# Kernel tuning notes

Hardware: AMD Instinct MI355X
Metric: run time of the kernel (lower is better)

## Reference

```python
import jax, jax.numpy as jnp
import numpy as np

BN_EPS = 1e-5
DIST_EPS = 1e-8
K = 3  # fixed 3-NN interpolation


def _cond_conv(x, t_embed, w_t, b_t, w_c, b_c, gamma, beta):
    # time conditioning: GELU(t) -> Linear -> add to channels
    te = jax.nn.gelu(t_embed, approximate=False) @ w_t.T + b_t  # (B, Cin)
    x = x + te[:, :, None]
    # kernel-size-1 Conv1d == channel GEMM
    x = jnp.einsum('oc,bcn->bon', w_c, x) + b_c[None, :, None]
    # BatchNorm1d, training mode: biased stats over (batch, length)
    m = jnp.mean(x, axis=(0, 2), keepdims=True)
    v = jnp.var(x, axis=(0, 2), keepdims=True)
    x = gamma[None, :, None] * (x - m) * jax.lax.rsqrt(v + BN_EPS) + beta[None, :, None]
    return jax.nn.gelu(x, approximate=False)


def _forward(xyz1, xyz2, points1, points2, t_embed,
             w_t1, b_t1, w_c1, b_c1, g1, be1,
             w_t2, b_t2, w_c2, b_c2, g2, be2):
    # squared euclidean distances (cdist**2), computed directly
    # d2[b,n,s] = ||xyz1[b,n]||^2 + ||xyz2[b,s]||^2 - 2 <xyz1[b,n], xyz2[b,s]>
    n1 = jnp.sum(xyz1 * xyz1, axis=-1)  # (B,N)
    n2 = jnp.sum(xyz2 * xyz2, axis=-1)  # (B,S)
    d2 = n1[:, :, None] + n2[:, None, :] - 2.0 * jnp.einsum('bnc,bsc->bns', xyz1, xyz2)
    # top-3 smallest distances (instead of wasteful full sort)
    neg, idx = jax.lax.top_k(-d2, K)        # (B,N,3)
    dists = -neg
    dist_recip = 1.0 / (dists + DIST_EPS)
    weight = dist_recip / jnp.sum(dist_recip, axis=2, keepdims=True)  # (B,N,3)
    pts2t = jnp.transpose(points2, (0, 2, 1))  # (B,S,C2)
    gathered = jax.vmap(lambda p, i: p[i])(pts2t, idx)  # (B,N,3,C2)
    interp = jnp.einsum('bnkc,bnk->bcn', gathered, weight)  # (B,C2,N)
    new_points = jnp.concatenate([points1, interp], axis=1)  # (B,C1+C2,N)
    new_points = _cond_conv(new_points, t_embed, w_t1, b_t1, w_c1, b_c1, g1, be1)
    new_points = _cond_conv(new_points, t_embed, w_t2, b_t2, w_c2, b_c2, g2, be2)
    return new_points


def setup_inputs() -> dict:
    key = jax.random.key(0)
    ks = jax.random.split(key, 12)
    B, N, S, C1, C2, T = 8, 8192, 2048, 128, 256, 256
    Cin = C1 + C2
    s = lambda fan: 1.0 / np.sqrt(fan)
    return {
        'xyz1': jax.random.normal(ks[0], (B, N, 3), jnp.float32),
        'xyz2': jax.random.normal(ks[1], (B, S, 3), jnp.float32),
        'points1': jax.random.normal(ks[2], (B, C1, N), jnp.float32),
        'points2': jax.random.normal(ks[3], (B, C2, S), jnp.float32),
        't_embed': jax.random.normal(ks[4], (B, T), jnp.float32),
        'w_t1': jax.random.normal(ks[5], (Cin, T), jnp.float32) * s(T),
        'b_t1': jnp.zeros((Cin,), jnp.float32),
        'w_c1': jax.random.normal(ks[6], (256, Cin), jnp.float32) * s(Cin),
        'b_c1': jnp.zeros((256,), jnp.float32),
        'g1': jnp.ones((256,), jnp.float32),
        'be1': jnp.zeros((256,), jnp.float32),
        'w_t2': jax.random.normal(ks[7], (256, T), jnp.float32) * s(T),
        'b_t2': jnp.zeros((256,), jnp.float32),
        'w_c2': jax.random.normal(ks[8], (256, 256), jnp.float32) * s(256),
        'b_c2': jnp.zeros((256,), jnp.float32),
        'g2': jnp.ones((256,), jnp.float32),
        'be2': jnp.zeros((256,), jnp.float32),
    }


def reference(xyz1, xyz2, points1, points2, t_embed,
              w_t1, b_t1, w_c1, b_c1, g1, be1,
              w_t2, b_t2, w_c2, b_c2, g2, be2):
    return _forward(xyz1, xyz2, points1, points2, t_embed,
                    w_t1, b_t1, w_c1, b_c1, g1, be1,
                    w_t2, b_t2, w_c2, b_c2, g2, be2)
```

## Files before the change

kernel.cpp:

```cpp
#include <hip/hip_runtime.h>
#include <cfloat>
#include <cmath>

#define B_   8
#define N_   8192
#define S_   2048
#define C1_  128
#define C2_  256
#define T_   256
#define CIN_ 384
#define CO_  256

#define KCH  16
#define KCS  (S_ / KCH)
#define KQB  1024

typedef __attribute__((ext_vector_type(8))) short short8;
typedef __attribute__((ext_vector_type(4))) float f32x4;

__device__ __forceinline__ float bf2f(unsigned short u) {
    union { unsigned int i; float f; } v; v.i = ((unsigned int)u) << 16; return v.f;
}
__device__ __forceinline__ unsigned short f2bf(float f) {
    union { float f; unsigned int i; } v; v.f = f;
    unsigned int i = v.i;
    unsigned int r = i + 0x7FFFu + ((i >> 16) & 1u);
    return (unsigned short)(r >> 16);
}
__device__ __forceinline__ float gelu_f(float x) {
    return 0.5f * x * (1.0f + erff(x * 0.70710678118654752440f));
}
__device__ __forceinline__ void async16(const void* g, void* l) {
    __builtin_amdgcn_global_load_lds((const __attribute__((address_space(1))) void*)g,
                                     (__attribute__((address_space(3))) void*)l, 16, 0, 0);
}

#define OFF_TE1   0u
#define OFF_TE2   16384u
#define OFF_BN1   28672u
#define OFF_BN2   30720u
#define OFF_WC1   1605632u
#define OFF_WC2   1802240u
#define OFF_P2T   2097152u
#define OFF_X1    10485760u
#define OFF_Y     60817408u
#define OFF_PD    OFF_Y
#define OFF_PI    (OFF_Y + 12582912u)
#define OFF_PS    OFF_P2T
#define OFF_PQ    (OFF_P2T + 1048576u)

__global__ __launch_bounds__(256) void prep_kernel(
    const float* __restrict__ w1, const float* __restrict__ w2,
    unsigned short* __restrict__ o1, unsigned short* __restrict__ o2,
    const float* __restrict__ t_embed,
    const float* __restrict__ w_t1, const float* __restrict__ b_t1,
    const float* __restrict__ w_t2, const float* __restrict__ b_t2,
    float* __restrict__ te1, float* __restrict__ te2)
{
    int bx = blockIdx.x, t = threadIdx.x;
    if (bx < 384) {
        int g = bx * 256 + t;
        o1[g] = f2bf(w1[g]);
        if (g < CO_ * CO_) o2[g] = f2bf(w2[g]);
        return;
    }
    __shared__ float gt[T_];
    int b = bx - 384;
    gt[t] = gelu_f(t_embed[b * T_ + t]);
    __syncthreads();
    for (int o = t; o < CIN_ + CO_; o += 256) {
        if (o < CIN_) {
            const float* w = w_t1 + o * T_;
            float s = 0.f;
            for (int k = 0; k < T_; ++k) s += gt[k] * w[k];
            te1[b * CIN_ + o] = s + b_t1[o];
        } else {
            int oo = o - CIN_;
            const float* w = w_t2 + oo * T_;
            float s = 0.f;
            for (int k = 0; k < T_; ++k) s += gt[k] * w[k];
            te2[b * CO_ + oo] = s + b_t2[oo];
        }
    }
}

__global__ __launch_bounds__(256) void knn_part_kernel(
    const float* __restrict__ xyz1, const float* __restrict__ xyz2,
    float* __restrict__ pd, int* __restrict__ pi)
{
    __shared__ float4 sp[KCS];
    int b = blockIdx.z, ch = blockIdx.y, tid = threadIdx.x;
    int s0 = ch * KCS;
    if (tid < KCS) {
        int gs = s0 + tid;
        float x = xyz2[(b * S_ + gs) * 3 + 0];
        float y = xyz2[(b * S_ + gs) * 3 + 1];
        float z = xyz2[(b * S_ + gs) * 3 + 2];
        sp[tid] = make_float4(x, y, z, x * x + y * y + z * z);
    }
    __syncthreads();

    float nx[4], ny[4], nz[4], nn[4];
    float d1[4], d2[4], d3[4];
    int   i1[4], i2[4], i3[4];
    #pragma unroll
    for (int qq = 0; qq < 4; ++qq) {
        int n = blockIdx.x * KQB + qq * 256 + tid;
        float x1 = xyz1[(b * N_ + n) * 3 + 0];
        float y1 = xyz1[(b * N_ + n) * 3 + 1];
        float z1 = xyz1[(b * N_ + n) * 3 + 2];
        nn[qq] = x1 * x1 + y1 * y1 + z1 * z1;
        nx[qq] = -2.0f * x1; ny[qq] = -2.0f * y1; nz[qq] = -2.0f * z1;
        d1[qq] = FLT_MAX; d2[qq] = FLT_MAX; d3[qq] = FLT_MAX;
        i1[qq] = 0; i2[qq] = 0; i3[qq] = 0;
    }

    for (int s = 0; s < KCS; s += 4) {
        #pragma unroll
        for (int u = 0; u < 4; ++u) {
            float4 p = sp[s + u];
            int gi = s0 + s + u;
            #pragma unroll
            for (int qq = 0; qq < 4; ++qq) {
                float d = fmaf(nx[qq], p.x,
                          fmaf(ny[qq], p.y,
                          fmaf(nz[qq], p.z, p.w)));
                bool c1 = d < d1[qq];
                bool c2 = d < d2[qq];
                bool c3 = d < d3[qq];
                float e1 = fminf(d1[qq], d);
                float e2 = __builtin_amdgcn_fmed3f(d1[qq], d2[qq], d);
                float e3 = __builtin_amdgcn_fmed3f(d2[qq], d3[qq], d);
                int u1  = c1 ? i1[qq] : gi;
                int n1i = c1 ? gi : i1[qq];
                int n2i = c2 ? u1 : i2[qq];
                int u2  = c2 ? i2[qq] : gi;
                int n3i = c3 ? u2 : i3[qq];
                d1[qq] = e1; d2[qq] = e2; d3[qq] = e3;
                i1[qq] = n1i; i2[qq] = n2i; i3[qq] = n3i;
            }
        }
    }

    #pragma unroll
    for (int qq = 0; qq < 4; ++qq) {
        int n = blockIdx.x * KQB + qq * 256 + tid;
        size_t pb = (((size_t)b * KCH + ch) * N_ + n) * 3;
        pd[pb + 0] = d1[qq] + nn[qq];
        pd[pb + 1] = d2[qq] + nn[qq];
        pd[pb + 2] = d3[qq] + nn[qq];
        pi[pb + 0] = i1[qq]; pi[pb + 1] = i2[qq]; pi[pb + 2] = i3[qq];
    }
}

__global__ __launch_bounds__(256) void transpose_fused(
    const float* __restrict__ p2, unsigned short* __restrict__ p2t,
    const float* __restrict__ p1, const float* __restrict__ te1,
    unsigned short* __restrict__ X1)
{
    __shared__ unsigned short tile[32][33];
    int bx = blockIdx.x;
    if (bx < 4096) {
        int b = bx >> 9, cy = (bx >> 6) & 7, sx = bx & 63;
        int s0 = sx * 32, c0 = cy * 32;
        #pragma unroll
        for (int j = 0; j < 4; ++j) {
            int c = threadIdx.y + j * 8;
            tile[c][threadIdx.x] = f2bf(p2[((size_t)b * C2_ + c0 + c) * S_ + s0 + threadIdx.x]);
        }
        __syncthreads();
        #pragma unroll
        for (int j = 0; j < 4; ++j) {
            int s = threadIdx.y + j * 8;
            p2t[((size_t)b * S_ + s0 + s) * C2_ + c0 + threadIdx.x] = tile[threadIdx.x][s];
        }
    } else {
        int bz = bx - 4096;
        int b = bz >> 10, cy = (bz >> 8) & 3, nx = bz & 255;
        int n0 = nx * 32, c0 = cy * 32;
        const float* te = te1 + b * CIN_;
        #pragma unroll
        for (int j = 0; j < 4; ++j) {
            int c = threadIdx.y + j * 8;
            tile[c][threadIdx.x] =
                f2bf(p1[((size_t)b * C1_ + c0 + c) * N_ + n0 + threadIdx.x] + te[c0 + c]);
        }
        __syncthreads();
        #pragma unroll
        for (int j = 0; j < 4; ++j) {
            int n = threadIdx.y + j * 8;
            X1[((size_t)b * N_ + n0 + n) * CIN_ + c0 + threadIdx.x] = tile[threadIdx.x][n];
        }
    }
}

__global__ __launch_bounds__(256) void interp2_kernel(
    const float* __restrict__ pd, const int* __restrict__ pi,
    const unsigned short* __restrict__ p2t,
    const float* __restrict__ te1, unsigned short* __restrict__ X1)
{
    __shared__ float spd[KCH][8][3];
    __shared__ int   spi[KCH][8][3];
    __shared__ float ste[C2_];
    int tid = threadIdx.x;
    int b = blockIdx.x >> 10;
    int n0 = (blockIdx.x & 1023) * 8;
    ste[tid] = te1[b * CIN_ + C1_ + tid];
    if (tid < 128) {
        int ch = tid >> 3, r = tid & 7;
        size_t pb = (((size_t)b * KCH + ch) * N_ + n0 + r) * 3;
        spd[ch][r][0] = pd[pb]; spd[ch][r][1] = pd[pb + 1]; spd[ch][r][2] = pd[pb + 2];
    } else {
        int t2 = tid - 128;
        int ch = t2 >> 3, r = t2 & 7;
        size_t pb = (((size_t)b * KCH + ch) * N_ + n0 + r) * 3;
        spi[ch][r][0] = pi[pb]; spi[ch][r][1] = pi[pb + 1]; spi[ch][r][2] = pi[pb + 2];
    }
    __syncthreads();

    int r = tid >> 5;
    int l = tid & 31;
    float d1, d2, d3; int i1, i2, i3;
    if (l < KCH) {
        d1 = spd[l][r][0]; d2 = spd[l][r][1]; d3 = spd[l][r][2];
        i1 = spi[l][r][0]; i2 = spi[l][r][1]; i3 = spi[l][r][2];
    } else {
        d1 = d2 = d3 = FLT_MAX;
        i1 = i2 = i3 = 0x7FFFFFFF;
    }
    #pragma unroll
    for (int m = 1; m <= 8; m <<= 1) {
        float pd1 = __shfl_xor(d1, m), pd2 = __shfl_xor(d2, m), pd3 = __shfl_xor(d3, m);
        int   pi1 = __shfl_xor(i1, m), pi2 = __shfl_xor(i2, m), pi3 = __shfl_xor(i3, m);
        #pragma unroll
        for (int k = 0; k < 3; ++k) {
            float d = (k == 0) ? pd1 : (k == 1) ? pd2 : pd3;
            int   i = (k == 0) ? pi1 : (k == 1) ? pi2 : pi3;
            bool c1 = (d < d1) || (d == d1 && i < i1);
            bool c2 = (d < d2) || (d == d2 && i < i2);
            bool c3 = (d < d3) || (d == d3 && i < i3);
            float e1 = c1 ? d : d1;        int j1 = c1 ? i : i1;
            float e2 = c1 ? d1 : (c2 ? d : d2);
            int   j2 = c1 ? i1 : (c2 ? i : i2);
            float e3 = c2 ? d2 : (c3 ? d : d3);
            int   j3 = c2 ? i2 : (c3 ? i : i3);
            d1 = e1; d2 = e2; d3 = e3; i1 = j1; i2 = j2; i3 = j3;
        }
    }
    int base = threadIdx.x & 32;
    d1 = __shfl(d1, base); d2 = __shfl(d2, base); d3 = __shfl(d3, base);
    i1 = __shfl(i1, base); i2 = __shfl(i2, base); i3 = __shfl(i3, base);
    float r1 = 1.0f / (d1 + 1e-8f);
    float r2 = 1.0f / (d2 + 1e-8f);
    float r3 = 1.0f / (d3 + 1e-8f);
    float rs = 1.0f / (r1 + r2 + r3);
    float w0 = r1 * rs, w1 = r2 * rs, w2 = r3 * rs;

    int gr = (b << 13) + n0 + r;
    int co = l * 8;
    const unsigned short* q0 = p2t + ((size_t)b * S_ + i1) * C2_ + co;
    const unsigned short* q1 = p2t + ((size_t)b * S_ + i2) * C2_ + co;
    const unsigned short* q2 = p2t + ((size_t)b * S_ + i3) * C2_ + co;
    union { short8 v; unsigned short u[8]; } a0, a1, a2, pk;
    a0.v = *(const short8*)q0;
    a1.v = *(const short8*)q1;
    a2.v = *(const short8*)q2;
    #pragma unroll
    for (int jj = 0; jj < 8; ++jj) {
        float v = w0 * bf2f(a0.u[jj]) + w1 * bf2f(a1.u[jj]) + w2 * bf2f(a2.u[jj])
                + ste[co + jj];
        pk.u[jj] = f2bf(v);
    }
    *(short8*)&X1[(size_t)gr * CIN_ + C1_ + co] = pk.v;
}

template <int K, int MODE>
__global__ __launch_bounds__(256) void gemm_bt(
    const unsigned short* __restrict__ A,
    const unsigned short* __restrict__ X,
    const float* __restrict__ bias,
    unsigned short* __restrict__ out,
    float* __restrict__ psum, float* __restrict__ psq)
{
    __shared__ unsigned short sA[128 * 64];
    __shared__ unsigned short sB[128 * 64];
    const int tid = threadIdx.x;
    const int lane = tid & 63, wave = tid >> 6;
    const int wo = wave >> 1, wm = wave & 1;
    const int quad = lane >> 4, col = lane & 15;
    const int b = blockIdx.z;
    const int x = blockIdx.x;
    const int perm = (x & 7) * 16 + (x >> 3);
    const int n_t = perm >> 1, o_t = perm & 1;
    const int o0 = o_t * 128;
    const int n0 = n_t * 128;
    const unsigned short* Xb = X + (size_t)b * N_ * K;
    const int prow = ((b << 6) + n_t) * 2 + wm;

    f32x4 acc[4][4];
    #pragma unroll
    for (int i = 0; i < 4; ++i)
        #pragma unroll
        for (int j = 0; j < 4; ++j) acc[i][j] = (f32x4){0.f, 0.f, 0.f, 0.f};

    for (int k0 = 0; k0 < K; k0 += 64) {
        #pragma unroll
        for (int i = 0; i < 4; ++i) {
            int chunk = i * 256 + tid;
            int row = chunk >> 3, c8 = chunk & 7;
            async16(&A [(o0 + row) * K + k0 + c8 * 8], &sA[chunk * 8]);
            async16(&Xb[(size_t)(n0 + row) * K + k0 + c8 * 8], &sB[chunk * 8]);
        }
        __syncthreads();
        #pragma unroll
        for (int kk = 0; kk < 64; kk += 32) {
            short8 af[4], bfr[4];
            #pragma unroll
            for (int i = 0; i < 4; ++i)
                af[i] = *(const short8*)&sA[(wo * 64 + i * 16 + col) * 64 + kk + quad * 8];
            #pragma unroll
            for (int j = 0; j < 4; ++j)
                bfr[j] = *(const short8*)&sB[(wm * 64 + j * 16 + col) * 64 + kk + quad * 8];
            #pragma unroll
            for (int i = 0; i < 4; ++i)
                #pragma unroll
                for (int j = 0; j < 4; ++j)
                    acc[i][j] = __builtin_amdgcn_mfma_f32_16x16x32_bf16(af[i], bfr[j], acc[i][j], 0, 0, 0);
        }
        __syncthreads();
    }

    #pragma unroll
    for (int i = 0; i < 4; ++i) {
        int oo = o0 + wo * 64 + i * 16 + quad * 4;
        float bv0 = bias[oo + 0], bv1 = bias[oo + 1];
        float bv2 = bias[oo + 2], bv3 = bias[oo + 3];
        float s0 = 0.f, s1 = 0.f, s2 = 0.f, s3 = 0.f;
        float q0 = 0.f, q1 = 0.f, q2 = 0.f, q3 = 0.f;
        #pragma unroll
        for (int j = 0; j < 4; ++j) {
            int nn = n0 + wm * 64 + j * 16 + col;
            float v0 = acc[i][j][0] + bv0, v1 = acc[i][j][1] + bv1;
            float v2 = acc[i][j][2] + bv2, v3 = acc[i][j][3] + bv3;
            s0 += v0; q0 += v0 * v0; s1 += v1; q1 += v1 * v1;
            s2 += v2; q2 += v2 * v2; s3 += v3; q3 += v3 * v3;
            if (MODE == 0) {
                union { unsigned short u[4]; uint2 p; } pk;
                pk.u[0] = f2bf(v0); pk.u[1] = f2bf(v1);
                pk.u[2] = f2bf(v2); pk.u[3] = f2bf(v3);
                *(uint2*)&out[((size_t)b * N_ + nn) * CO_ + oo] = pk.p;
            } else {
                out[((size_t)b * CO_ + oo + 0) * N_ + nn] = f2bf(v0);
                out[((size_t)b * CO_ + oo + 1) * N_ + nn] = f2bf(v1);
                out[((size_t)b * CO_ + oo + 2) * N_ + nn] = f2bf(v2);
                out[((size_t)b * CO_ + oo + 3) * N_ + nn] = f2bf(v3);
            }
        }
        #pragma unroll
        for (int off = 1; off < 16; off <<= 1) {
            s0 += __shfl_down(s0, off); q0 += __shfl_down(q0, off);
            s1 += __shfl_down(s1, off); q1 += __shfl_down(q1, off);
            s2 += __shfl_down(s2, off); q2 += __shfl_down(q2, off);
            s3 += __shfl_down(s3, off); q3 += __shfl_down(q3, off);
        }
        if (col == 0) {
            float* ps = psum + (size_t)oo * 1024 + prow;
            float* pq = psq  + (size_t)oo * 1024 + prow;
            ps[0] = s0; ps[1024] = s1; ps[2048] = s2; ps[3072] = s3;
            pq[0] = q0; pq[1024] = q1; pq[2048] = q2; pq[3072] = q3;
        }
    }
}

__global__ __launch_bounds__(256) void bn_reduce_kernel(
    const float* __restrict__ psum, const float* __restrict__ psq,
    const float* __restrict__ gamma, const float* __restrict__ beta,
    float* __restrict__ scale, float* __restrict__ shift)
{
    int ch = blockIdx.x * 8 + (threadIdx.x >> 5);
    int l = threadIdx.x & 31;
    float s = 0.f, q = 0.f;
    for (int r = l; r < 1024; r += 32) {
        s += psum[(size_t)ch * 1024 + r];
        q += psq [(size_t)ch * 1024 + r];
    }
    #pragma unroll
    for (int off = 16; off > 0; off >>= 1) {
        s += __shfl_down(s, off, 32);
        q += __shfl_down(q, off, 32);
    }
    if (l == 0) {
        const float inv = 1.0f / 65536.0f;
        float m = s * inv;
        float var = fmaxf(q * inv - m * m, 0.f);
        float sc = gamma[ch] / sqrtf(var + 1e-5f);
        scale[ch] = sc;
        shift[ch] = beta[ch] - m * sc;
    }
}

__global__ __launch_bounds__(256) void apply1_kernel(
    unsigned short* __restrict__ y, const float* __restrict__ scale,
    const float* __restrict__ shift, const float* __restrict__ te2)
{
    __shared__ float ssc[CO_], ssh[CO_], ste[CO_];
    int b = blockIdx.x >> 10;
    int t = threadIdx.x;
    ssc[t] = scale[t]; ssh[t] = shift[t]; ste[t] = te2[b * CO_ + t];
    __syncthreads();
    int g = blockIdx.x * 256 + t;
    int row = g >> 5;
    int og = (g & 31) * 8;
    unsigned short* p = y + (size_t)row * CO_ + og;
    union { short8 v; unsigned short u[8]; } in, op;
    in.v = *(short8*)p;
    #pragma unroll
    for (int jj = 0; jj < 8; ++jj) {
        int o = og + jj;
        op.u[jj] = f2bf(gelu_f(ssc[o] * bf2f(in.u[jj]) + ssh[o]) + ste[o]);
    }
    *(short8*)p = op.v;
}

__global__ __launch_bounds__(256) void final_kernel(
    const unsigned short* __restrict__ z, const float* __restrict__ scale,
    const float* __restrict__ shift, float* __restrict__ out)
{
    int g = blockIdx.x * 256 + threadIdx.x;
    size_t e = (size_t)g * 8;
    int row = (int)(e >> 13);
    int o = row & (CO_ - 1);
    float sc = scale[o], sh = shift[o];
    union { short8 v; unsigned short u[8]; } in;
    in.v = *(const short8*)&z[e];
    float vo[8];
    #pragma unroll
    for (int jj = 0; jj < 8; ++jj)
        vo[jj] = gelu_f(sc * bf2f(in.u[jj]) + sh);
    *(float4*)&out[e]     = make_float4(vo[0], vo[1], vo[2], vo[3]);
    *(float4*)&out[e + 4] = make_float4(vo[4], vo[5], vo[6], vo[7]);
}

extern "C" void kernel_launch(void* const* d_in, const int* in_sizes, int n_in,
                              void* d_out, int out_size, void* d_ws, size_t ws_size,
                              hipStream_t stream)
{
    (void)in_sizes; (void)n_in; (void)out_size; (void)ws_size;
    const float* xyz1    = (const float*)d_in[0];
    const float* xyz2    = (const float*)d_in[1];
    const float* points1 = (const float*)d_in[2];
    const float* points2 = (const float*)d_in[3];
    const float* t_embed = (const float*)d_in[4];
    const float* w_t1    = (const float*)d_in[5];
    const float* b_t1    = (const float*)d_in[6];
    const float* w_c1    = (const float*)d_in[7];
    const float* b_c1    = (const float*)d_in[8];
    const float* g1      = (const float*)d_in[9];
    const float* be1     = (const float*)d_in[10];
    const float* w_t2    = (const float*)d_in[11];
    const float* b_t2    = (const float*)d_in[12];
    const float* w_c2    = (const float*)d_in[13];
    const float* b_c2    = (const float*)d_in[14];
    const float* g2      = (const float*)d_in[15];
    const float* be2     = (const float*)d_in[16];

    char* w = (char*)d_ws;
    float* te1        = (float*)(w + OFF_TE1);
    float* te2        = (float*)(w + OFF_TE2);
    float* scale1     = (float*)(w + OFF_BN1);
    float* shift1     = scale1 + 256;
    float* scale2     = (float*)(w + OFF_BN2);
    float* shift2     = scale2 + 256;
    unsigned short* wc1 = (unsigned short*)(w + OFF_WC1);
    unsigned short* wc2 = (unsigned short*)(w + OFF_WC2);
    unsigned short* p2t = (unsigned short*)(w + OFF_P2T);
    float* pd         = (float*)(w + OFF_PD);
    int*   pi         = (int*)(w + OFF_PI);
    float* psum       = (float*)(w + OFF_PS);
    float* psq        = (float*)(w + OFF_PQ);
    unsigned short* X1  = (unsigned short*)(w + OFF_X1);
    unsigned short* Z   = (unsigned short*)(w + OFF_X1);
    unsigned short* Y   = (unsigned short*)(w + OFF_Y);
    float* out = (float*)d_out;

    hipLaunchKernelGGL(prep_kernel, dim3(392), dim3(256), 0, stream,
                       w_c1, w_c2, wc1, wc2, t_embed, w_t1, b_t1, w_t2, b_t2, te1, te2);
    hipLaunchKernelGGL(knn_part_kernel, dim3(N_ / KQB, KCH, B_), dim3(256), 0, stream,
                       xyz1, xyz2, pd, pi);
    hipLaunchKernelGGL(transpose_fused, dim3(12288), dim3(32, 8), 0, stream,
                       points2, p2t, points1, te1, X1);
    hipLaunchKernelGGL(interp2_kernel, dim3(B_ * N_ / 8), dim3(256), 0, stream,
                       pd, pi, p2t, te1, X1);
    hipLaunchKernelGGL((gemm_bt<CIN_, 0>), dim3(128, 1, B_), dim3(256), 0, stream,
                       wc1, X1, b_c1, Y, psum, psq);
    hipLaunchKernelGGL(bn_reduce_kernel, dim3(32), dim3(256), 0, stream,
                       psum, psq, g1, be1, scale1, shift1);
    hipLaunchKernelGGL(apply1_kernel, dim3(8192), dim3(256), 0, stream,
                       Y, scale1, shift1, te2);
    hipLaunchKernelGGL((gemm_bt<CO_, 1>), dim3(128, 1, B_), dim3(256), 0, stream,
                       wc2, Y, b_c2, Z, psum, psq);
    hipLaunchKernelGGL(bn_reduce_kernel, dim3(32), dim3(256), 0, stream,
                       psum, psq, g2, be2, scale2, shift2);
    hipLaunchKernelGGL(final_kernel, dim3(8192), dim3(256), 0, stream,
                       Z, scale2, shift2, out);
}
```

Before: 347.5 us.

## Fuse BN1-apply/GELU into second GEMM B-load and retune KNN partitioning

Removes the standalone apply1 kernel and instead applies BN1 scale/shift, GELU and the time embedding while staging Y tiles into shared memory inside a new gemm2_fused kernel. This drops one full read and write pass over the intermediate activation. It also halves the KNN split count and the queries per block, which shrinks the partial top-3 buffers and merge shuffles, and swaps the med3 builtin for inline asm. In exchange, the B operand now loads synchronously with per-element erf work in the GEMM loop, and GELU is recomputed once for each of the two output-channel tiles.

```diff
diff --git a/kernel.cpp b/kernel.cpp
--- a/kernel.cpp
+++ b/kernel.cpp
@@ -11,9 +11,9 @@
 #define CIN_ 384
 #define CO_  256
 
-#define KCH  16
+#define KCH  8
 #define KCS  (S_ / KCH)
-#define KQB  1024
+#define KQB  512
 
 typedef __attribute__((ext_vector_type(8))) short short8;
 typedef __attribute__((ext_vector_type(4))) float f32x4;
@@ -33,6 +33,11 @@
 __device__ __forceinline__ void async16(const void* g, void* l) {
     __builtin_amdgcn_global_load_lds((const __attribute__((address_space(1))) void*)g,
                                      (__attribute__((address_space(3))) void*)l, 16, 0, 0);
+}
+__device__ __forceinline__ float med3f(float a, float b, float c) {
+    float r;
+    asm("v_med3_f32 %0, %1, %2, %3" : "=v"(r) : "v"(a), "v"(b), "v"(c));
+    return r;
 }
 
 #define OFF_TE1   0u
@@ -45,7 +50,7 @@
 #define OFF_X1    10485760u
 #define OFF_Y     60817408u
 #define OFF_PD    OFF_Y
-#define OFF_PI    (OFF_Y + 12582912u)
+#define OFF_PI    (OFF_Y + 6291456u)
 #define OFF_PS    OFF_P2T
 #define OFF_PQ    (OFF_P2T + 1048576u)
 
@@ -91,7 +96,7 @@
     __shared__ float4 sp[KCS];
     int b = blockIdx.z, ch = blockIdx.y, tid = threadIdx.x;
     int s0 = ch * KCS;
-    if (tid < KCS) {
+    {
         int gs = s0 + tid;
         float x = xyz2[(b * S_ + gs) * 3 + 0];
         float y = xyz2[(b * S_ + gs) * 3 + 1];
@@ -100,11 +105,11 @@
     }
     __syncthreads();
 
-    float nx[4], ny[4], nz[4], nn[4];
-    float d1[4], d2[4], d3[4];
-    int   i1[4], i2[4], i3[4];
-    #pragma unroll
-    for (int qq = 0; qq < 4; ++qq) {
+    float nx[2], ny[2], nz[2], nn[2];
+    float d1[2], d2[2], d3[2];
+    int   i1[2], i2[2], i3[2];
+    #pragma unroll
+    for (int qq = 0; qq < 2; ++qq) {
         int n = blockIdx.x * KQB + qq * 256 + tid;
         float x1 = xyz1[(b * N_ + n) * 3 + 0];
         float y1 = xyz1[(b * N_ + n) * 3 + 1];
@@ -121,7 +126,7 @@
             float4 p = sp[s + u];
             int gi = s0 + s + u;
             #pragma unroll
-            for (int qq = 0; qq < 4; ++qq) {
+            for (int qq = 0; qq < 2; ++qq) {
                 float d = fmaf(nx[qq], p.x,
                           fmaf(ny[qq], p.y,
                           fmaf(nz[qq], p.z, p.w)));
@@ -129,8 +134,8 @@
                 bool c2 = d < d2[qq];
                 bool c3 = d < d3[qq];
                 float e1 = fminf(d1[qq], d);
-                float e2 = __builtin_amdgcn_fmed3f(d1[qq], d2[qq], d);
-                float e3 = __builtin_amdgcn_fmed3f(d2[qq], d3[qq], d);
+                float e2 = med3f(d1[qq], d2[qq], d);
+                float e3 = med3f(d2[qq], d3[qq], d);
                 int u1  = c1 ? i1[qq] : gi;
                 int n1i = c1 ? gi : i1[qq];
                 int n2i = c2 ? u1 : i2[qq];
@@ -143,7 +148,7 @@
     }
 
     #pragma unroll
-    for (int qq = 0; qq < 4; ++qq) {
+    for (int qq = 0; qq < 2; ++qq) {
         int n = blockIdx.x * KQB + qq * 256 + tid;
         size_t pb = (((size_t)b * KCH + ch) * N_ + n) * 3;
         pd[pb + 0] = d1[qq] + nn[qq];
@@ -206,12 +211,12 @@
     int b = blockIdx.x >> 10;
     int n0 = (blockIdx.x & 1023) * 8;
     ste[tid] = te1[b * CIN_ + C1_ + tid];
-    if (tid < 128) {
+    if (tid < 64) {
         int ch = tid >> 3, r = tid & 7;
         size_t pb = (((size_t)b * KCH + ch) * N_ + n0 + r) * 3;
         spd[ch][r][0] = pd[pb]; spd[ch][r][1] = pd[pb + 1]; spd[ch][r][2] = pd[pb + 2];
-    } else {
-        int t2 = tid - 128;
+    } else if (tid < 128) {
+        int t2 = tid - 64;
         int ch = t2 >> 3, r = t2 & 7;
         size_t pb = (((size_t)b * KCH + ch) * N_ + n0 + r) * 3;
         spi[ch][r][0] = pi[pb]; spi[ch][r][1] = pi[pb + 1]; spi[ch][r][2] = pi[pb + 2];
@@ -229,7 +234,7 @@
         i1 = i2 = i3 = 0x7FFFFFFF;
     }
     #pragma unroll
-    for (int m = 1; m <= 8; m <<= 1) {
+    for (int m = 1; m <= 4; m <<= 1) {
         float pd1 = __shfl_xor(d1, m), pd2 = __shfl_xor(d2, m), pd3 = __shfl_xor(d3, m);
         int   pi1 = __shfl_xor(i1, m), pi2 = __shfl_xor(i2, m), pi3 = __shfl_xor(i3, m);
         #pragma unroll
@@ -372,6 +377,116 @@
     }
 }
 
+__global__ __launch_bounds__(256) void gemm2_fused(
+    const unsigned short* __restrict__ A,
+    const unsigned short* __restrict__ Y,
+    const float* __restrict__ bias,
+    const float* __restrict__ scale1, const float* __restrict__ shift1,
+    const float* __restrict__ te2,
+    unsigned short* __restrict__ out,
+    float* __restrict__ psum, float* __restrict__ psq)
+{
+    const int K = CO_;
+    __shared__ unsigned short sA[128 * 64];
+    __shared__ unsigned short sB[128 * 64];
+    __shared__ float ssc[CO_], ssh[CO_], ste[CO_];
+    const int tid = threadIdx.x;
+    const int lane = tid & 63, wave = tid >> 6;
+    const int wo = wave >> 1, wm = wave & 1;
+    const int quad = lane >> 4, col = lane & 15;
+    const int b = blockIdx.z;
+    const int x = blockIdx.x;
+    const int perm = (x & 7) * 16 + (x >> 3);
+    const int n_t = perm >> 1, o_t = perm & 1;
+    const int o0 = o_t * 128;
+    const int n0 = n_t * 128;
+    const unsigned short* Yb = Y + (size_t)b * N_ * K;
+    const int prow = ((b << 6) + n_t) * 2 + wm;
+
+    ssc[tid] = scale1[tid]; ssh[tid] = shift1[tid]; ste[tid] = te2[b * CO_ + tid];
+    __syncthreads();
+
+    f32x4 acc[4][4];
+    #pragma unroll
+    for (int i = 0; i < 4; ++i)
+        #pragma unroll
+        for (int j = 0; j < 4; ++j) acc[i][j] = (f32x4){0.f, 0.f, 0.f, 0.f};
+
+    for (int k0 = 0; k0 < K; k0 += 64) {
+        #pragma unroll
+        for (int i = 0; i < 4; ++i) {
+            int chunk = i * 256 + tid;
+            int row = chunk >> 3, c8 = chunk & 7;
+            async16(&A[(o0 + row) * K + k0 + c8 * 8], &sA[chunk * 8]);
+        }
+        #pragma unroll
+        for (int i = 0; i < 4; ++i) {
+            int chunk = i * 256 + tid;
+            int row = chunk >> 3, c8 = chunk & 7;
+            int cbase = k0 + c8 * 8;
+            union { short8 v; unsigned short u[8]; } raw, pk;
+            raw.v = *(const short8*)&Yb[(size_t)(n0 + row) * K + cbase];
+            #pragma unroll
+            for (int jj = 0; jj < 8; ++jj) {
+                int c = cbase + jj;
+                pk.u[jj] = f2bf(gelu_f(ssc[c] * bf2f(raw.u[jj]) + ssh[c]) + ste[c]);
+            }
+            *(short8*)&sB[chunk * 8] = pk.v;
+        }
+        __syncthreads();
+        #pragma unroll
+        for (int kk = 0; kk < 64; kk += 32) {
+            short8 af[4], bfr[4];
+            #pragma unroll
+            for (int i = 0; i < 4; ++i)
+                af[i] = *(const short8*)&sA[(wo * 64 + i * 16 + col) * 64 + kk + quad * 8];
+            #pragma unroll
+            for (int j = 0; j < 4; ++j)
+                bfr[j] = *(const short8*)&sB[(wm * 64 + j * 16 + col) * 64 + kk + quad * 8];
+            #pragma unroll
+            for (int i = 0; i < 4; ++i)
+                #pragma unroll
+                for (int j = 0; j < 4; ++j)
+                    acc[i][j] = __builtin_amdgcn_mfma_f32_16x16x32_bf16(af[i], bfr[j], acc[i][j], 0, 0, 0);
+        }
+        __syncthreads();
+    }
+
+    #pragma unroll
+    for (int i = 0; i < 4; ++i) {
+        int oo = o0 + wo * 64 + i * 16 + quad * 4;
+        float bv0 = bias[oo + 0], bv1 = bias[oo + 1];
+        float bv2 = bias[oo + 2], bv3 = bias[oo + 3];
+        float s0 = 0.f, s1 = 0.f, s2 = 0.f, s3 = 0.f;
+        float q0 = 0.f, q1 = 0.f, q2 = 0.f, q3 = 0.f;
+        #pragma unroll
+        for (int j = 0; j < 4; ++j) {
+            int nn = n0 + wm * 64 + j * 16 + col;
+            float v0 = acc[i][j][0] + bv0, v1 = acc[i][j][1] + bv1;
+            float v2 = acc[i][j][2] + bv2, v3 = acc[i][j][3] + bv3;
+            s0 += v0; q0 += v0 * v0; s1 += v1; q1 += v1 * v1;
+            s2 += v2; q2 += v2 * v2; s3 += v3; q3 += v3 * v3;
+            out[((size_t)b * CO_ + oo + 0) * N_ + nn] = f2bf(v0);
+            out[((size_t)b * CO_ + oo + 1) * N_ + nn] = f2bf(v1);
+            out[((size_t)b * CO_ + oo + 2) * N_ + nn] = f2bf(v2);
+            out[((size_t)b * CO_ + oo + 3) * N_ + nn] = f2bf(v3);
+        }
+        #pragma unroll
+        for (int off = 1; off < 16; off <<= 1) {
+            s0 += __shfl_down(s0, off); q0 += __shfl_down(q0, off);
+            s1 += __shfl_down(s1, off); q1 += __shfl_down(q1, off);
+            s2 += __shfl_down(s2, off); q2 += __shfl_down(q2, off);
+            s3 += __shfl_down(s3, off); q3 += __shfl_down(q3, off);
+        }
+        if (col == 0) {
+            float* ps = psum + (size_t)oo * 1024 + prow;
+            float* pq = psq  + (size_t)oo * 1024 + prow;
+            ps[0] = s0; ps[1024] = s1; ps[2048] = s2; ps[3072] = s3;
+            pq[0] = q0; pq[1024] = q1; pq[2048] = q2; pq[3072] = q3;
+        }
+    }
+}
+
 __global__ __launch_bounds__(256) void bn_reduce_kernel(
     const float* __restrict__ psum, const float* __restrict__ psq,
     const float* __restrict__ gamma, const float* __restrict__ beta,
@@ -397,29 +512,6 @@
         scale[ch] = sc;
         shift[ch] = beta[ch] - m * sc;
     }
-}
-
-__global__ __launch_bounds__(256) void apply1_kernel(
-    unsigned short* __restrict__ y, const float* __restrict__ scale,
-    const float* __restrict__ shift, const float* __restrict__ te2)
-{
-    __shared__ float ssc[CO_], ssh[CO_], ste[CO_];
-    int b = blockIdx.x >> 10;
-    int t = threadIdx.x;
-    ssc[t] = scale[t]; ssh[t] = shift[t]; ste[t] = te2[b * CO_ + t];
-    __syncthreads();
-    int g = blockIdx.x * 256 + t;
-    int row = g >> 5;
-    int og = (g & 31) * 8;
-    unsigned short* p = y + (size_t)row * CO_ + og;
-    union { short8 v; unsigned short u[8]; } in, op;
-    in.v = *(short8*)p;
-    #pragma unroll
-    for (int jj = 0; jj < 8; ++jj) {
-        int o = og + jj;
-        op.u[jj] = f2bf(gelu_f(ssc[o] * bf2f(in.u[jj]) + ssh[o]) + ste[o]);
-    }
-    *(short8*)p = op.v;
 }
 
 __global__ __launch_bounds__(256) void final_kernel(
@@ -495,10 +587,8 @@
                        wc1, X1, b_c1, Y, psum, psq);
     hipLaunchKernelGGL(bn_reduce_kernel, dim3(32), dim3(256), 0, stream,
                        psum, psq, g1, be1, scale1, shift1);
-    hipLaunchKernelGGL(apply1_kernel, dim3(8192), dim3(256), 0, stream,
-                       Y, scale1, shift1, te2);
-    hipLaunchKernelGGL((gemm_bt<CO_, 1>), dim3(128, 1, B_), dim3(256), 0, stream,
-                       wc2, Y, b_c2, Z, psum, psq);
+    hipLaunchKernelGGL(gemm2_fused, dim3(128, 1, B_), dim3(256), 0, stream,
+                       wc2, Y, b_c2, scale1, shift1, te2, Z, psum, psq);
     hipLaunchKernelGGL(bn_reduce_kernel, dim3(32), dim3(256), 0, stream,
                        psum, psq, g2, be2, scale2, shift2);
     hipLaunchKernelGGL(final_kernel, dim3(8192), dim3(256), 0, stream,
```

After: 357.4 us. 2.8% more time.
